# Performance work log

Hardware: AMD Instinct MI355X
Metric: run time of the kernel (lower is better)

## Reference

```python
import jax, jax.numpy as jnp
import numpy as np

N = 1024          # num_features
H = N // 2        # core dimension (num_params // 2)
NB = 4            # num_blocks
B = 16384         # batch


def _lifted_core(rot_params, diag_params):
    """Build the (N, N) lifted core matrix for one Cayley block."""
    # skew-symmetric matrix from the H rotation params
    S = rot_params[:, None] - rot_params[None, :]            # (H, H)
    I = jnp.eye(H, dtype=rot_params.dtype)
    rotation = jnp.linalg.solve(I - S, I + S)                # Cayley transform
    core = diag_params[:, None] * rotation                   # diag(d) @ rotation
    # rot90(core, k=o) only depends on o mod 4 -> precompute 4 variants
    rots = jnp.stack([core,
                      jnp.rot90(core, 1),
                      jnp.rot90(core, 2),
                      jnp.rot90(core, 3)])                   # (4, H, H)

    def body(lifted, o):
        blk = jax.lax.dynamic_slice(lifted, (o, o), (H, H)) + rots[o % 4]
        return jax.lax.dynamic_update_slice(lifted, blk, (o, o)), None

    lifted, _ = jax.lax.scan(body, jnp.zeros((N, N), dtype=core.dtype),
                             jnp.arange(H + 1))
    return lifted


def setup_inputs() -> dict:
    key = jax.random.key(0)
    ks = jax.random.split(key, 5)
    x = jax.random.normal(ks[0], (B, N), dtype=jnp.float32)
    enc_rot = jax.random.normal(ks[1], (NB, H), dtype=jnp.float32)
    enc_diag = jax.random.normal(ks[2], (NB, H), dtype=jnp.float32)
    dec_rot = jax.random.normal(ks[3], (NB, H), dtype=jnp.float32)
    dec_diag = jax.random.normal(ks[4], (NB, H), dtype=jnp.float32)
    return {"x": x, "enc_rot": enc_rot, "enc_diag": enc_diag,
            "dec_rot": dec_rot, "dec_diag": dec_diag}


def reference(x, enc_rot, enc_diag, dec_rot, dec_diag):
    s = x
    for i in range(NB):                                      # encoder blocks
        s = s @ _lifted_core(enc_rot[i], enc_diag[i]).T
    bottleneck = s
    out = s
    for i in range(NB):                                      # decoder blocks
        out = out @ _lifted_core(dec_rot[i], dec_diag[i]).T
    return bottleneck, out
```

## Files before the change

### kernel.cpp

```cpp
#include <hip/hip_runtime.h>
#include <hip/hip_bf16.h>
#include <cstdint>
#include <cstddef>

#define H 512
#define NFEAT 1024
#define BATCH 16384
#define LM ((size_t)1 << 20)
#define KOP 576

using bf16 = __hip_bfloat16;
using bf16x8 = __attribute__((ext_vector_type(8))) __bf16;
using f32x4 = __attribute__((ext_vector_type(4))) float;
using f32x16 = __attribute__((ext_vector_type(16))) float;

__device__ __forceinline__ void gload16(void* lds, const void* g) {
  __builtin_amdgcn_global_load_lds(
      (__attribute__((address_space(1))) void*)g,
      (__attribute__((address_space(3))) void*)lds,
      16, 0, 0);
}

__global__ void prep_kernel(const float* __restrict__ er, const float* __restrict__ ed,
                            const float* __restrict__ dr, const float* __restrict__ dd,
                            float* __restrict__ ab) {
  const int mat = blockIdx.x;
  const int lane = threadIdx.x;
  const float* u = (mat < 4) ? (er + mat * H) : (dr + (mat - 4) * H);
  const float* d = (mat < 4) ? (ed + mat * H) : (dd + (mat - 4) * H);

  double s = 0.0, q = 0.0;
  for (int k = 0; k < 8; ++k) {
    double v = (double)u[lane + 64 * k];
    s += v;
    q += v * v;
  }
  for (int off = 32; off; off >>= 1) {
    s += __shfl_down(s, off);
    q += __shfl_down(q, off);
  }
  s = __shfl(s, 0);
  q = __shfl(q, 0);

  const double det = 1.0 - s * s + (double)H * q;
  const double cuv = 2.0 * (1.0 + s) / det;
  const double cuu = -2.0 * (double)H / det;
  const double cvv = -2.0 * q / det;
  const double cvu = -2.0 * (1.0 - s) / det;

  float* a = ab + mat * 1024;
  float* b = a + H;
  for (int k = 0; k < 8; ++k) {
    int idx = lane + 64 * k;
    double ui = (double)u[idx], di = (double)d[idx];
    a[idx] = (float)(di * (cuv * ui + cvv));
    b[idx] = (float)(di * (cuu * ui + cvu));
  }
}

__global__ __launch_bounds__(256) void prep2_kernel(
    const float* __restrict__ er, const float* __restrict__ ed,
    const float* __restrict__ dr, const float* __restrict__ dd,
    const float* __restrict__ ab, float* __restrict__ Tpref) {
  __shared__ float buf[4][512];
  __shared__ float tmp[4][512];
  const int mat = blockIdx.x;
  const float* d = (mat < 4) ? (ed + mat * H) : (dd + (mat - 4) * H);
  const float* a = ab + mat * 1024;
  const int t = threadIdx.x;
  for (int m = t; m < 512; m += 256) {
    buf[0][m] = a[m];
    buf[1][m] = a[511 - m];
    buf[2][m] = d[m];
    buf[3][m] = d[511 - m];
  }
  __syncthreads();
  for (int s = 4; s <= 256; s <<= 1) {
    for (int m = t; m < 512; m += 256)
#pragma unroll
      for (int q = 0; q < 4; ++q) tmp[q][m] = (m >= s) ? buf[q][m - s] : 0.f;
    __syncthreads();
    for (int m = t; m < 512; m += 256)
#pragma unroll
      for (int q = 0; q < 4; ++q) buf[q][m] += tmp[q][m];
    __syncthreads();
  }
  float* tp = Tpref + mat * 2048;
  for (int m = t; m < 512; m += 256) {
    tp[m] = buf[0][m];
    tp[512 + m] = buf[1][m];
    tp[1024 + m] = buf[2][m];
    tp[1536 + m] = buf[3][m];
  }
}

__global__ __launch_bounds__(256) void genops_kernel(
    const float* __restrict__ er, const float* __restrict__ dr,
    const float* __restrict__ ab,
    bf16* __restrict__ Ah, bf16* __restrict__ Al,
    bf16* __restrict__ Bh, bf16* __restrict__ Bl) {
  const int x = blockIdx.x;
  const int mat = blockIdx.y;
  const float* u = (mat < 4) ? (er + mat * H) : (dr + (mat - 4) * H);
  const float* b = ab + mat * 1024 + H;
  const int t = threadIdx.x;
  const size_t base = ((size_t)mat * 1024 + x) * KOP;
  for (int k = t; k < KOP; k += 256) {
    float av = 0.f, bv = 0.f;
    if (k <= 128) {
      const int o = 4 * k;
      const int ia = x - o;
      av = (ia >= 0 && ia < 512) ? b[ia] : 0.f;
      bv = (ia >= 0 && ia < 512) ? u[ia] : 0.f;
    } else if (k <= 256) {
      const int o = 4 * (k - 129) + 1;
      const int ia = 511 - x + o;
      const int ib = x - o;
      av = (ia >= 0 && ia < 512) ? u[ia] : 0.f;
      bv = (ib >= 0 && ib < 512) ? b[ib] : 0.f;
    } else if (k <= 384) {
      const int o = 4 * (k - 257) + 2;
      const int ia = 511 - x + o;
      av = (ia >= 0 && ia < 512) ? b[ia] : 0.f;
      bv = (ia >= 0 && ia < 512) ? u[ia] : 0.f;
    } else if (k <= 512) {
      const int o = 4 * (k - 385) + 3;
      const int ia = x - o;
      const int ib = 511 - x + o;
      av = (ia >= 0 && ia < 512) ? u[ia] : 0.f;
      bv = (ib >= 0 && ib < 512) ? b[ib] : 0.f;
    }
    const bf16 ah = __float2bfloat16(av);
    Ah[base + k] = ah;
    Al[base + k] = __float2bfloat16(av - __bfloat162float(ah));
    const bf16 bh = __float2bfloat16(bv);
    Bh[base + k] = bh;
    Bl[base + k] = __float2bfloat16(bv - __bfloat162float(bh));
  }
}

__global__ __launch_bounds__(256) void buildgemm_kernel(
    const bf16* __restrict__ Ah, const bf16* __restrict__ Al,
    const bf16* __restrict__ Bh, const bf16* __restrict__ Bl,
    const float* __restrict__ ed, const float* __restrict__ dd,
    const float* __restrict__ Tpref, bf16* __restrict__ Lbase) {
  __shared__ __align__(16) bf16 smem[4 * 8192];
  __shared__ float pa[512], parev[512], pd[512], pdrev[512], sdl[512];
  bf16* sAh = smem;
  bf16* sAl = smem + 8192;
  bf16* sBh = smem + 16384;
  bf16* sBl = smem + 24576;

  const int tid = threadIdx.x;
  const int lane = tid & 63;
  const int wave = tid >> 6;
  const int wr = wave >> 1;
  const int wc = wave & 1;
  const int mat = blockIdx.z;
  const int row0 = blockIdx.x * 128;
  const int col0 = blockIdx.y * 128;

  {
    const float* tp = Tpref + mat * 2048;
    const float* d = (mat < 4) ? (ed + mat * H) : (dd + (mat - 4) * H);
    for (int m = tid; m < 512; m += 256) {
      pa[m] = tp[m];
      parev[m] = tp[512 + m];
      pd[m] = tp[1024 + m];
      pdrev[m] = tp[1536 + m];
      sdl[m] = d[m];
    }
  }

  const size_t OPS = (size_t)mat * 1024 * KOP;
  const int srow = tid >> 3;
  const int sce = (((tid * 16) ^ (((tid >> 3) & 7) << 4)) & 127) >> 1;
  const size_t abase = OPS + (size_t)(row0 + srow) * KOP + sce;
  const size_t bbase = OPS + (size_t)(col0 + srow) * KOP + sce;
  const int dst0 = tid * 8;

  f32x16 acc[2][2] = {};

  for (int kt = 0; kt < 9; ++kt) {
    const int k0 = kt * 64;
#pragma unroll
    for (int q = 0; q < 4; ++q) {
      const size_t ga = abase + (size_t)(32 * q) * KOP + k0;
      const size_t gb = bbase + (size_t)(32 * q) * KOP + k0;
      const int dq = q * 2048 + dst0;
      gload16(sAh + dq, Ah + ga);
      gload16(sAl + dq, Al + ga);
      gload16(sBh + dq, Bh + gb);
      gload16(sBl + dq, Bl + gb);
    }
    __syncthreads();

    const int l31 = lane & 31;
    const int kh16 = (lane >> 5) * 16;
#pragma unroll
    for (int ks = 0; ks < 4; ++ks) {
      bf16x8 fah[2], fal[2], fbh[2], fbl[2];
#pragma unroll
      for (int m = 0; m < 2; ++m) {
        const int arow = wr * 64 + m * 32 + l31;
        const int abk = (arow * 128 + ks * 32 + kh16) ^ ((arow & 7) << 4);
        fah[m] = *(const bf16x8*)((const char*)sAh + abk);
        fal[m] = *(const bf16x8*)((const char*)sAl + abk);
        const int brow = wc * 64 + m * 32 + l31;
        const int bbk = (brow * 128 + ks * 32 + kh16) ^ ((brow & 7) << 4);
        fbh[m] = *(const bf16x8*)((const char*)sBh + bbk);
        fbl[m] = *(const bf16x8*)((const char*)sBl + bbk);
      }
#pragma unroll
      for (int m = 0; m < 2; ++m)
#pragma unroll
        for (int n = 0; n < 2; ++n) {
          acc[m][n] = __builtin_amdgcn_mfma_f32_32x32x16_bf16(fah[m], fbh[n], acc[m][n], 0, 0, 0);
          acc[m][n] = __builtin_amdgcn_mfma_f32_32x32x16_bf16(fah[m], fbl[n], acc[m][n], 0, 0, 0);
          acc[m][n] = __builtin_amdgcn_mfma_f32_32x32x16_bf16(fal[m], fbh[n], acc[m][n], 0, 0, 0);
        }
    }
    __syncthreads();
  }

  auto apart = [&](int i, int j) -> float {
    const int lo = max(0, max(i, j) - 511);
    const int hi = min(512, min(i, j));
    if (lo > hi) return 0.f;
    float v = 0.f;
    {
      int o1 = lo + ((0 - lo) & 3), o2 = hi - (hi & 3);
      if (o1 <= o2) { int mx = i - o1, mn = i - o2; v += pa[mx] - (mn >= 4 ? pa[mn - 4] : 0.f); }
    }
    {
      int o1 = lo + ((1 - lo) & 3), o2 = hi - ((hi - 1) & 3);
      if (o1 <= o2) { int mx = j - o1, mn = j - o2; v += pa[mx] - (mn >= 4 ? pa[mn - 4] : 0.f); }
    }
    {
      int o1 = lo + ((2 - lo) & 3), o2 = hi - ((hi - 2) & 3);
      if (o1 <= o2) { int mx = i - o1, mn = i - o2; v += parev[mx] - (mn >= 4 ? parev[mn - 4] : 0.f); }
    }
    {
      int o1 = lo + ((3 - lo) & 3), o2 = hi - ((hi - 3) & 3);
      if (o1 <= o2) { int mx = j - o1, mn = j - o2; v += parev[mx] - (mn >= 4 ? parev[mn - 4] : 0.f); }
    }
    if (i == j) {
      {
        int o1 = lo + ((0 - lo) & 3), o2 = hi - (hi & 3);
        if (o1 <= o2) { int mx = i - o1, mn = i - o2; v += pd[mx] - (mn >= 4 ? pd[mn - 4] : 0.f); }
      }
      {
        int o1 = lo + ((2 - lo) & 3), o2 = hi - ((hi - 2) & 3);
        if (o1 <= o2) { int mx = i - o1, mn = i - o2; v += pdrev[mx] - (mn >= 4 ? pdrev[mn - 4] : 0.f); }
      }
    }
    const int m2 = i + j - 511;
    if (m2 >= 0 && !(m2 & 1)) {
      const int os = m2 >> 1;
      if (os >= lo && os <= hi) {
        const int r = os & 3;
        if (r == 1) v += sdl[j - os];
        else if (r == 3) v += sdl[511 - (j - os)];
      }
    }
    return v;
  };

  const int ocol0 = col0 + wc * 64 + (lane & 31);
  const int rb = (lane >> 5) << 2;
#pragma unroll
  for (int m = 0; m < 2; ++m)
#pragma unroll
    for (int n = 0; n < 2; ++n)
#pragma unroll
      for (int r = 0; r < 16; ++r) {
        const int grow = row0 + wr * 64 + m * 32 + (r & 3) + ((r >> 2) << 3) + rb;
        const int gcol = ocol0 + n * 32;
        const float v = acc[m][n][r] + apart(grow, gcol);
        const size_t off = ((size_t)mat << 21) + ((size_t)grow << 10) + (size_t)gcol;
        const bf16 hb = __float2bfloat16(v);
        Lbase[off] = hb;
        Lbase[off + LM] = __float2bfloat16(v - __bfloat162float(hb));
      }
}

__global__ void splith_kernel(const float* __restrict__ x, bf16* __restrict__ h) {
  const int n4 = BATCH * NFEAT / 4;
  int idx = blockIdx.x * blockDim.x + threadIdx.x;
  int stride = gridDim.x * blockDim.x;
  for (int i = idx; i < n4; i += stride) {
    float4 v = ((const float4*)x)[i];
    union { bf16 b[4]; short4 s; } Hu;
    Hu.b[0] = __float2bfloat16(v.x);
    Hu.b[1] = __float2bfloat16(v.y);
    Hu.b[2] = __float2bfloat16(v.z);
    Hu.b[3] = __float2bfloat16(v.w);
    ((short4*)h)[i] = Hu.s;
  }
}

struct TPtrs { const bf16* s; bf16* d; };
struct T6 { TPtrs t[6]; };

__global__ __launch_bounds__(256) void transposeB_kernel(T6 p) {
  const bf16* S = p.t[blockIdx.z].s;
  bf16* D = p.t[blockIdx.z].d;
  __shared__ ushort tile[64][68];
  const int i0 = blockIdx.x * 64, j0 = blockIdx.y * 64;
  const int tid = threadIdx.x;
  const int rr = tid >> 4;
  const int cc = (tid & 15) * 4;
#pragma unroll
  for (int it = 0; it < 4; ++it) {
    const int row = it * 16 + rr;
    const size_t so = (size_t)(i0 + row) * 1024 + j0 + cc;
    ushort4 v = *(const ushort4*)((const ushort*)S + so);
    tile[row][cc] = v.x; tile[row][cc + 1] = v.y;
    tile[row][cc + 2] = v.z; tile[row][cc + 3] = v.w;
  }
  __syncthreads();
#pragma unroll
  for (int it = 0; it < 4; ++it) {
    const int row = it * 16 + rr;
    ushort4 o;
    o.x = tile[cc][row];     o.y = tile[cc + 1][row];
    o.z = tile[cc + 2][row]; o.w = tile[cc + 3][row];
    const size_t dofs = (size_t)(j0 + row) * 1024 + i0 + cc;
    *(ushort4*)((ushort*)D + dofs) = o;
  }
}

struct GPtrs { const bf16* a; const bf16* b; bf16* yh; bf16* yl; };
struct G4 { GPtrs g[4]; };

__global__ __launch_bounds__(256) void chaingemm4_kernel(G4 p) {
  GPtrs q = p.g[blockIdx.z];
  const bf16* A = q.a;
  const bf16* Bh = q.b;
  const bf16* Bl = q.b + LM;

  __shared__ __align__(16) bf16 smem[2 * 3 * 4096];

  const int tid = threadIdx.x;
  const int lane = tid & 63;
  const int wave = tid >> 6;
  const int wr = wave >> 1, wc = wave & 1;
  const int r0 = blockIdx.x * 64, c0 = blockIdx.y * 64;

  const int srow = tid >> 3;
  const int scol = (((tid & 7) ^ (srow & 7))) * 8;
  const int dst = tid * 8;
  const size_t ga0 = (size_t)(r0 + srow) * 1024 + scol;
  const size_t gb0 = (size_t)(c0 + srow) * 1024 + scol;

  auto STAGE = [&](int nb, int k0) {
    bf16* base = smem + nb * 12288;
    gload16(base + dst,        A + ga0 + k0);
    gload16(base + 2048 + dst, A + ga0 + 32 * 1024 + k0);
    gload16(base + 4096 + dst,        Bh + gb0 + k0);
    gload16(base + 4096 + 2048 + dst, Bh + gb0 + 32 * 1024 + k0);
    gload16(base + 8192 + dst,        Bl + gb0 + k0);
    gload16(base + 8192 + 2048 + dst, Bl + gb0 + 32 * 1024 + k0);
  };

  const int l31 = lane & 31;
  const int klg = lane >> 5;
  const int ar = wr * 32 + l31;
  const int br = wc * 32 + l31;
  int aoff[4], boff[4];
#pragma unroll
  for (int ks = 0; ks < 4; ++ks) {
    const int lgA = (ks << 1) | klg;
    aoff[ks] = ar * 64 + ((lgA ^ (ar & 7)) << 3);
    boff[ks] = br * 64 + ((lgA ^ (br & 7)) << 3);
  }

  f32x16 acc = {};

  STAGE(0, 0);
  asm volatile("s_waitcnt vmcnt(0)" ::: "memory");
  __builtin_amdgcn_s_barrier();

  for (int t = 0; t < 16; ++t) {
    const int buf = t & 1;
    const int nb = buf ^ 1;
    const bool pf = (t < 15);
    if (pf) STAGE(nb, (t + 1) * 64);

    const bf16* pA = smem + buf * 12288;
    const bf16* pBh = pA + 4096;
    const bf16* pBl = pA + 8192;
#pragma unroll
    for (int ks = 0; ks < 4; ++ks) {
      bf16x8 ah = *(const bf16x8*)(pA + aoff[ks]);
      bf16x8 bh = *(const bf16x8*)(pBh + boff[ks]);
      bf16x8 bl = *(const bf16x8*)(pBl + boff[ks]);
      acc = __builtin_amdgcn_mfma_f32_32x32x16_bf16(ah, bh, acc, 0, 0, 0);
      acc = __builtin_amdgcn_mfma_f32_32x32x16_bf16(ah, bl, acc, 0, 0, 0);
    }
    if (pf) asm volatile("s_waitcnt vmcnt(0)" ::: "memory");
    __builtin_amdgcn_s_barrier();
  }

  const int oc = c0 + wc * 32 + l31;
  const int rb = (lane >> 5) << 2;
#pragma unroll
  for (int r = 0; r < 16; ++r) {
    const int gr = r0 + wr * 32 + (r & 3) + ((r >> 2) << 3) + rb;
    const size_t off = (size_t)gr * 1024 + oc;
    const float v = acc[r];
    const bf16 hb = __float2bfloat16(v);
    q.yh[off] = hb;
    q.yl[off] = __float2bfloat16(v - __bfloat162float(hb));
  }
}

__global__ __launch_bounds__(512, 1) void gemmbig_kernel(
    const bf16* __restrict__ A, const bf16* __restrict__ Bh_,
    float* __restrict__ Y0, float* __restrict__ Y1) {
  __shared__ __align__(16) bf16 smem[2 * 2 * 8192];

  const int tid = threadIdx.x;
  const int lane = tid & 63;
  const int wave = tid >> 6;
  const int wr = wave >> 2;
  const int wc = wave & 3;

  const int pdisp = blockIdx.x + (blockIdx.y << 6);
  const int xcd = pdisp & 7;
  const int chk = pdisp >> 3;
  const int row0 = (xcd * 8 + (chk >> 3)) * 256;
  const int col0 = (chk & 7) * 256;

  const int gsrc = (tid & 3) ^ ((tid >> 3) & 3);
  const int dst = tid * 8;
  const size_t abase = (size_t)(row0 + (tid >> 2)) * NFEAT + gsrc * 8;
  const size_t bbase = (size_t)(col0 + (tid >> 2)) * NFEAT + gsrc * 8;

  auto STAGE2 = [&](int nb, int arr, const bf16* __restrict__ src, size_t base, int k0) {
    bf16* d = smem + nb * 16384 + arr * 8192 + dst;
    gload16(d, src + base + k0);
    gload16(d + 4096, src + base + 131072 + k0);
  };

  const int l31 = lane & 31;
  const int hb = lane >> 5;
  int aoffB[4][2], boffB[2][2];
#pragma unroll
  for (int m = 0; m < 4; ++m) {
    const int r = wr * 128 + m * 32 + l31;
#pragma unroll
    for (int ks = 0; ks < 2; ++ks)
      aoffB[m][ks] = r * 64 + ((((ks << 1) | hb) ^ ((r >> 1) & 3)) << 4);
  }
#pragma unroll
  for (int n = 0; n < 2; ++n) {
    const int r = wc * 64 + n * 32 + l31;
#pragma unroll
    for (int ks = 0; ks < 2; ++ks)
      boffB[n][ks] = r * 64 + ((((ks << 1) | hb) ^ ((r >> 1) & 3)) << 4);
  }

  auto LD = [](const char* base, int off) { return *(const bf16x8*)(base + off); };

  f32x16 acc[4][2] = {};

  STAGE2(0, 0, A, abase, 0);
  STAGE2(0, 1, Bh_, bbase, 0);
  asm volatile("s_waitcnt vmcnt(0)" ::: "memory");
  __builtin_amdgcn_s_barrier();

  for (int t = 0; t < 32; ++t) {
    const int buf = t & 1;
    const int nb = buf ^ 1;
    const int k1 = (t + 1) * 32;
    const char* pA = (const char*)(smem + buf * 16384);
    const char* pBh = pA + 16384;
    const bool pf = (t < 31);

    bf16x8 ga[2][2], fbh[2][2];

    if (pf) {
      STAGE2(nb, 0, A, abase, k1);
      STAGE2(nb, 1, Bh_, bbase, k1);
    }
#pragma unroll
    for (int mi = 0; mi < 2; ++mi)
#pragma unroll
      for (int ks = 0; ks < 2; ++ks)
        ga[mi][ks] = LD(pA, aoffB[mi][ks]);
#pragma unroll
    for (int n = 0; n < 2; ++n)
#pragma unroll
      for (int ks = 0; ks < 2; ++ks)
        fbh[n][ks] = LD(pBh, boffB[n][ks]);
    __builtin_amdgcn_s_barrier();
    __builtin_amdgcn_s_setprio(1);
#pragma unroll
    for (int ks = 0; ks < 2; ++ks)
#pragma unroll
      for (int mi = 0; mi < 2; ++mi)
#pragma unroll
        for (int n = 0; n < 2; ++n)
          acc[mi][n] = __builtin_amdgcn_mfma_f32_32x32x16_bf16(ga[mi][ks], fbh[n][ks], acc[mi][n], 0, 0, 0);
    __builtin_amdgcn_s_setprio(0);
    __builtin_amdgcn_s_barrier();

#pragma unroll
    for (int mi = 0; mi < 2; ++mi)
#pragma unroll
      for (int ks = 0; ks < 2; ++ks)
        ga[mi][ks] = LD(pA, aoffB[2 + mi][ks]);
    __builtin_amdgcn_s_barrier();
    __builtin_amdgcn_s_setprio(1);
#pragma unroll
    for (int ks = 0; ks < 2; ++ks)
#pragma unroll
      for (int mi = 0; mi < 2; ++mi)
#pragma unroll
        for (int n = 0; n < 2; ++n)
          acc[2 + mi][n] = __builtin_amdgcn_mfma_f32_32x32x16_bf16(ga[mi][ks], fbh[n][ks], acc[2 + mi][n], 0, 0, 0);
    __builtin_amdgcn_s_setprio(0);
    if (pf) asm volatile("s_waitcnt vmcnt(0)" ::: "memory");
    __builtin_amdgcn_s_barrier();
  }

  float* Yb = (col0 < 1024) ? Y0 : (Y1 - 1024);
  const int ocol0 = col0 + wc * 64 + l31;
  const int rb = (lane >> 5) << 2;
#pragma unroll
  for (int m = 0; m < 4; ++m)
#pragma unroll
    for (int n = 0; n < 2; ++n)
#pragma unroll
      for (int r = 0; r < 16; ++r) {
        const int grow = row0 + wr * 128 + m * 32 + (r & 3) + ((r >> 2) << 3) + rb;
        const int gcol = ocol0 + n * 32;
        Yb[(size_t)grow * NFEAT + (size_t)gcol] = acc[m][n][r];
      }
}

extern "C" void kernel_launch(void* const* d_in, const int* in_sizes, int n_in,
                              void* d_out, int out_size, void* d_ws, size_t ws_size,
                              hipStream_t stream) {
  (void)in_sizes; (void)n_in; (void)out_size; (void)ws_size;
  const float* x  = (const float*)d_in[0];
  const float* er = (const float*)d_in[1];
  const float* ed = (const float*)d_in[2];
  const float* dr = (const float*)d_in[3];
  const float* dd = (const float*)d_in[4];

  float* O0 = (float*)d_out;
  float* O1 = O0 + (size_t)BATCH * NFEAT;

  bf16* Lb = (bf16*)d_ws;
  float* ab = (float*)(Lb + 16 * LM);
  bf16* Qh = (bf16*)(ab + 8 * 1024);

  float* Tpref = O0;
  bf16* SB = (bf16*)((char*)O0 + (1 << 20));
  auto slot = [&](int s) { return SB + (size_t)s * LM; };

  const size_t OPN = (size_t)8 * 1024 * KOP;
  bf16* Aoph = (bf16*)O1;
  bf16* Aopl = Aoph + OPN;
  bf16* Boph = Aopl + OPN;
  bf16* Bopl = Boph + OPN;

  prep_kernel<<<8, 64, 0, stream>>>(er, ed, dr, dd, ab);
  prep2_kernel<<<8, 256, 0, stream>>>(er, ed, dr, dd, ab, Tpref);
  genops_kernel<<<dim3(1024, 8), 256, 0, stream>>>(er, dr, ab, Aoph, Aopl, Boph, Bopl);
  buildgemm_kernel<<<dim3(8, 8, 8), 256, 0, stream>>>(Aoph, Aopl, Boph, Bopl,
                                                      ed, dd, Tpref, Lb);
  splith_kernel<<<4096, 256, 0, stream>>>(x, Qh);

  {
    T6 p;
    p.t[0] = {Lb + 0 * LM,  slot(0)};
    p.t[1] = {Lb + 4 * LM,  slot(2)};
    p.t[2] = {Lb + 5 * LM,  slot(3)};
    p.t[3] = {Lb + 8 * LM,  slot(4)};
    p.t[4] = {Lb + 12 * LM, slot(6)};
    p.t[5] = {Lb + 13 * LM, slot(7)};
    transposeB_kernel<<<dim3(16, 16, 6), 256, 0, stream>>>(p);
  }
  {
    G4 p;
    p.g[0] = {slot(0),      Lb + 2 * LM,  slot(8),  slot(9)};
    p.g[1] = {Lb + 6 * LM,  slot(2),      slot(10), slot(11)};
    p.g[2] = {slot(4),      Lb + 10 * LM, slot(12), slot(13)};
    p.g[3] = {Lb + 14 * LM, slot(6),      slot(14), slot(15)};
    chaingemm4_kernel<<<dim3(16, 16, 4), 256, 0, stream>>>(p);
  }
  {
    G4 p;
    p.g[0] = {slot(8),  slot(10), slot(0), slot(1)};
    p.g[1] = {slot(12), slot(14), slot(2), slot(3)};
    p.g[2] = p.g[0];
    p.g[3] = p.g[1];
    chaingemm4_kernel<<<dim3(16, 16, 2), 256, 0, stream>>>(p);
  }
  {
    T6 p;
    p.t[0] = {slot(0), Lb + 0 * LM};
    p.t[1] = {slot(2), Lb + 2 * LM};
    p.t[2] = p.t[0]; p.t[3] = p.t[0]; p.t[4] = p.t[0]; p.t[5] = p.t[0];
    transposeB_kernel<<<dim3(16, 16, 2), 256, 0, stream>>>(p);
  }
  {
    G4 p;
    p.g[0] = {Lb + 2 * LM, slot(0), Lb + 1 * LM, slot(4)};
    p.g[1] = p.g[0]; p.g[2] = p.g[0]; p.g[3] = p.g[0];
    chaingemm4_kernel<<<dim3(16, 16, 1), 256, 0, stream>>>(p);
  }

  gemmbig_kernel<<<dim3(64, 8), 512, 0, stream>>>(Qh, Lb, O0, O1);
}
```

Before: 259.3 us.

## Triple-buffer LDS in big GEMM and drop intra-iteration barriers

Moves the big GEMM kernel from double- to triple-buffered LDS staging, prefetching two K-steps ahead and waiting with vmcnt(4) so one tile's loads stay in flight across iterations. It also removes the two mid-iteration barriers and keeps a single barrier per K-step. This is meant to hide global load latency better and cut synchronisation stalls. The cost is 50% more LDS (96 KB per block) and reliance on vmcnt ordering for correctness.

```diff
diff --git a/kernel.cpp b/kernel.cpp
--- a/kernel.cpp
+++ b/kernel.cpp
@@ -418,7 +418,7 @@
 __global__ __launch_bounds__(512, 1) void gemmbig_kernel(
     const bf16* __restrict__ A, const bf16* __restrict__ Bh_,
     float* __restrict__ Y0, float* __restrict__ Y1) {
-  __shared__ __align__(16) bf16 smem[2 * 2 * 8192];
+  __shared__ __align__(16) bf16 smem[3 * 2 * 8192];
 
   const int tid = threadIdx.x;
   const int lane = tid & 63;
@@ -437,10 +437,11 @@
   const size_t abase = (size_t)(row0 + (tid >> 2)) * NFEAT + gsrc * 8;
   const size_t bbase = (size_t)(col0 + (tid >> 2)) * NFEAT + gsrc * 8;
 
-  auto STAGE2 = [&](int nb, int arr, const bf16* __restrict__ src, size_t base, int k0) {
-    bf16* d = smem + nb * 16384 + arr * 8192 + dst;
-    gload16(d, src + base + k0);
-    gload16(d + 4096, src + base + 131072 + k0);
+  auto STAGE = [&](bf16* bufp, int k0) {
+    gload16(bufp + dst, A + abase + k0);
+    gload16(bufp + 4096 + dst, A + abase + 131072 + k0);
+    gload16(bufp + 8192 + dst, Bh_ + bbase + k0);
+    gload16(bufp + 12288 + dst, Bh_ + bbase + 131072 + k0);
   };
 
   const int l31 = lane & 31;
@@ -465,36 +466,33 @@
 
   f32x16 acc[4][2] = {};
 
-  STAGE2(0, 0, A, abase, 0);
-  STAGE2(0, 1, Bh_, bbase, 0);
-  asm volatile("s_waitcnt vmcnt(0)" ::: "memory");
+  bf16* b0 = smem;
+  bf16* b1 = smem + 16384;
+  bf16* b2 = smem + 32768;
+
+  STAGE(b0, 0);
+  STAGE(b1, 32);
+  asm volatile("s_waitcnt vmcnt(4)" ::: "memory");
   __builtin_amdgcn_s_barrier();
 
   for (int t = 0; t < 32; ++t) {
-    const int buf = t & 1;
-    const int nb = buf ^ 1;
-    const int k1 = (t + 1) * 32;
-    const char* pA = (const char*)(smem + buf * 16384);
+    if (t < 30) STAGE(b2, (t + 2) * 32);
+
+    const char* pA = (const char*)b0;
     const char* pBh = pA + 16384;
-    const bool pf = (t < 31);
 
     bf16x8 ga[2][2], fbh[2][2];
-
-    if (pf) {
-      STAGE2(nb, 0, A, abase, k1);
-      STAGE2(nb, 1, Bh_, bbase, k1);
-    }
+#pragma unroll
+    for (int n = 0; n < 2; ++n)
+#pragma unroll
+      for (int ks = 0; ks < 2; ++ks)
+        fbh[n][ks] = LD(pBh, boffB[n][ks]);
 #pragma unroll
     for (int mi = 0; mi < 2; ++mi)
 #pragma unroll
       for (int ks = 0; ks < 2; ++ks)
         ga[mi][ks] = LD(pA, aoffB[mi][ks]);
-#pragma unroll
-    for (int n = 0; n < 2; ++n)
-#pragma unroll
-      for (int ks = 0; ks < 2; ++ks)
-        fbh[n][ks] = LD(pBh, boffB[n][ks]);
-    __builtin_amdgcn_s_barrier();
+
     __builtin_amdgcn_s_setprio(1);
 #pragma unroll
     for (int ks = 0; ks < 2; ++ks)
@@ -504,14 +502,13 @@
         for (int n = 0; n < 2; ++n)
           acc[mi][n] = __builtin_amdgcn_mfma_f32_32x32x16_bf16(ga[mi][ks], fbh[n][ks], acc[mi][n], 0, 0, 0);
     __builtin_amdgcn_s_setprio(0);
-    __builtin_amdgcn_s_barrier();
 
 #pragma unroll
     for (int mi = 0; mi < 2; ++mi)
 #pragma unroll
       for (int ks = 0; ks < 2; ++ks)
         ga[mi][ks] = LD(pA, aoffB[2 + mi][ks]);
-    __builtin_amdgcn_s_barrier();
+
     __builtin_amdgcn_s_setprio(1);
 #pragma unroll
     for (int ks = 0; ks < 2; ++ks)
@@ -521,8 +518,15 @@
         for (int n = 0; n < 2; ++n)
           acc[2 + mi][n] = __builtin_amdgcn_mfma_f32_32x32x16_bf16(ga[mi][ks], fbh[n][ks], acc[2 + mi][n], 0, 0, 0);
     __builtin_amdgcn_s_setprio(0);
-    if (pf) asm volatile("s_waitcnt vmcnt(0)" ::: "memory");
+
+    if (t < 30) {
+      asm volatile("s_waitcnt vmcnt(4)" ::: "memory");
+    } else {
+      asm volatile("s_waitcnt vmcnt(0)" ::: "memory");
+    }
     __builtin_amdgcn_s_barrier();
+
+    bf16* tmp = b0; b0 = b1; b1 = b2; b2 = tmp;
   }
 
   float* Yb = (col0 < 1024) ? Y0 : (Y1 - 1024);
```

New measurement: 258.3 us. No clear change (-0.4%).

## Deepen gemmbig LDS pipeline to four stages and switch to 16x16x32 MFMA

Applied to the files above, without the earlier changes.

Replaces the double-buffered LDS pipeline in the big GEMM with a four-buffer ring that prefetches three K-steps ahead. The A and B global-to-LDS loads for each step are split across the two compute halves, and partial vmcnt waits are used. It also moves from 32x32x16 to 16x16x32 MFMA fragments, with new swizzled LDS offsets and a matching output mapping. The aim is to hide global load latency better, at the cost of twice the LDS and more fragment loads per step.

```diff
diff --git a/kernel.cpp b/kernel.cpp
--- a/kernel.cpp
+++ b/kernel.cpp
@@ -418,7 +418,7 @@
 __global__ __launch_bounds__(512, 1) void gemmbig_kernel(
     const bf16* __restrict__ A, const bf16* __restrict__ Bh_,
     float* __restrict__ Y0, float* __restrict__ Y1) {
-  __shared__ __align__(16) bf16 smem[2 * 2 * 8192];
+  __shared__ __align__(16) bf16 smem[4 * 16384];
 
   const int tid = threadIdx.x;
   const int lane = tid & 63;
@@ -432,111 +432,104 @@
   const int row0 = (xcd * 8 + (chk >> 3)) * 256;
   const int col0 = (chk & 7) * 256;
 
-  const int gsrc = (tid & 3) ^ ((tid >> 3) & 3);
+  const int sr = tid >> 2;
+  const int sc = ((tid & 3) ^ ((tid >> 3) & 3)) * 8;
+  const size_t abase0 = (size_t)(row0 + sr) * NFEAT + sc;
+  const size_t abase1 = (size_t)(row0 + sr + 128) * NFEAT + sc;
+  const size_t bbase0 = (size_t)(col0 + sr) * NFEAT + sc;
+  const size_t bbase1 = (size_t)(col0 + sr + 128) * NFEAT + sc;
   const int dst = tid * 8;
-  const size_t abase = (size_t)(row0 + (tid >> 2)) * NFEAT + gsrc * 8;
-  const size_t bbase = (size_t)(col0 + (tid >> 2)) * NFEAT + gsrc * 8;
-
-  auto STAGE2 = [&](int nb, int arr, const bf16* __restrict__ src, size_t base, int k0) {
-    bf16* d = smem + nb * 16384 + arr * 8192 + dst;
-    gload16(d, src + base + k0);
-    gload16(d + 4096, src + base + 131072 + k0);
+
+  auto STAGE_A = [&](int buf, int k0) {
+    bf16* base = smem + buf * 16384;
+    gload16(base + dst, A + abase0 + k0);
+    gload16(base + 4096 + dst, A + abase1 + k0);
   };
-
-  const int l31 = lane & 31;
-  const int hb = lane >> 5;
-  int aoffB[4][2], boffB[2][2];
-#pragma unroll
-  for (int m = 0; m < 4; ++m) {
-    const int r = wr * 128 + m * 32 + l31;
-#pragma unroll
-    for (int ks = 0; ks < 2; ++ks)
-      aoffB[m][ks] = r * 64 + ((((ks << 1) | hb) ^ ((r >> 1) & 3)) << 4);
-  }
-#pragma unroll
-  for (int n = 0; n < 2; ++n) {
-    const int r = wc * 64 + n * 32 + l31;
-#pragma unroll
-    for (int ks = 0; ks < 2; ++ks)
-      boffB[n][ks] = r * 64 + ((((ks << 1) | hb) ^ ((r >> 1) & 3)) << 4);
-  }
-
-  auto LD = [](const char* base, int off) { return *(const bf16x8*)(base + off); };
-
-  f32x16 acc[4][2] = {};
-
-  STAGE2(0, 0, A, abase, 0);
-  STAGE2(0, 1, Bh_, bbase, 0);
-  asm volatile("s_waitcnt vmcnt(0)" ::: "memory");
+  auto STAGE_B = [&](int buf, int k0) {
+    bf16* base = smem + buf * 16384 + 8192;
+    gload16(base + dst, Bh_ + bbase0 + k0);
+    gload16(base + 4096 + dst, Bh_ + bbase1 + k0);
+  };
+
+  const int l15 = lane & 15;
+  const int kg16 = (lane >> 4) * 16;
+  const int swz = ((l15 >> 1) & 3) << 4;
+  const int kcol = kg16 ^ swz;
+  int aoff[8], boff[4];
+#pragma unroll
+  for (int fr = 0; fr < 8; ++fr)
+    aoff[fr] = (wr * 128 + fr * 16 + l15) * 64 + kcol;
+#pragma unroll
+  for (int fc = 0; fc < 4; ++fc)
+    boff[fc] = (wc * 64 + fc * 16 + l15) * 64 + kcol + 16384;
+
+  auto LD = [&](int buf, int off) {
+    return *(const bf16x8*)((const char*)(smem + buf * 16384) + off);
+  };
+
+  f32x4 acc[8][4] = {};
+
+  STAGE_A(0, 0); STAGE_B(0, 0);
+  STAGE_A(1, 32); STAGE_B(1, 32);
+  STAGE_A(2, 64); STAGE_B(2, 64);
+  asm volatile("s_waitcnt vmcnt(8)" ::: "memory");
   __builtin_amdgcn_s_barrier();
 
-  for (int t = 0; t < 32; ++t) {
-    const int buf = t & 1;
-    const int nb = buf ^ 1;
-    const int k1 = (t + 1) * 32;
-    const char* pA = (const char*)(smem + buf * 16384);
-    const char* pBh = pA + 16384;
-    const bool pf = (t < 31);
-
-    bf16x8 ga[2][2], fbh[2][2];
-
-    if (pf) {
-      STAGE2(nb, 0, A, abase, k1);
-      STAGE2(nb, 1, Bh_, bbase, k1);
-    }
-#pragma unroll
-    for (int mi = 0; mi < 2; ++mi)
-#pragma unroll
-      for (int ks = 0; ks < 2; ++ks)
-        ga[mi][ks] = LD(pA, aoffB[mi][ks]);
-#pragma unroll
-    for (int n = 0; n < 2; ++n)
-#pragma unroll
-      for (int ks = 0; ks < 2; ++ks)
-        fbh[n][ks] = LD(pBh, boffB[n][ks]);
+  for (int T = 0; T < 32; ++T) {
+    const int buf = T & 3;
+    const int kpre = (T + 3) * 32;
+    const bool pf = (T < 29);
+
+    bf16x8 fa[4], fb[4];
+
+    if (pf) STAGE_A((T + 3) & 3, kpre);
+#pragma unroll
+    for (int fc = 0; fc < 4; ++fc) fb[fc] = LD(buf, boff[fc]);
+#pragma unroll
+    for (int fr = 0; fr < 4; ++fr) fa[fr] = LD(buf, aoff[fr]);
     __builtin_amdgcn_s_barrier();
     __builtin_amdgcn_s_setprio(1);
 #pragma unroll
-    for (int ks = 0; ks < 2; ++ks)
-#pragma unroll
-      for (int mi = 0; mi < 2; ++mi)
-#pragma unroll
-        for (int n = 0; n < 2; ++n)
-          acc[mi][n] = __builtin_amdgcn_mfma_f32_32x32x16_bf16(ga[mi][ks], fbh[n][ks], acc[mi][n], 0, 0, 0);
+    for (int fr = 0; fr < 4; ++fr)
+#pragma unroll
+      for (int fc = 0; fc < 4; ++fc)
+        acc[fr][fc] = __builtin_amdgcn_mfma_f32_16x16x32_bf16(fa[fr], fb[fc], acc[fr][fc], 0, 0, 0);
     __builtin_amdgcn_s_setprio(0);
     __builtin_amdgcn_s_barrier();
 
-#pragma unroll
-    for (int mi = 0; mi < 2; ++mi)
-#pragma unroll
-      for (int ks = 0; ks < 2; ++ks)
-        ga[mi][ks] = LD(pA, aoffB[2 + mi][ks]);
+    if (pf) STAGE_B((T + 3) & 3, kpre);
+#pragma unroll
+    for (int fr = 0; fr < 4; ++fr) fa[fr] = LD(buf, aoff[4 + fr]);
     __builtin_amdgcn_s_barrier();
     __builtin_amdgcn_s_setprio(1);
 #pragma unroll
-    for (int ks = 0; ks < 2; ++ks)
-#pragma unroll
-      for (int mi = 0; mi < 2; ++mi)
-#pragma unroll
-        for (int n = 0; n < 2; ++n)
-          acc[2 + mi][n] = __builtin_amdgcn_mfma_f32_32x32x16_bf16(ga[mi][ks], fbh[n][ks], acc[2 + mi][n], 0, 0, 0);
+    for (int fr = 0; fr < 4; ++fr)
+#pragma unroll
+      for (int fc = 0; fc < 4; ++fc)
+        acc[4 + fr][fc] = __builtin_amdgcn_mfma_f32_16x16x32_bf16(fa[fr], fb[fc], acc[4 + fr][fc], 0, 0, 0);
     __builtin_amdgcn_s_setprio(0);
-    if (pf) asm volatile("s_waitcnt vmcnt(0)" ::: "memory");
+    if (T <= 28) {
+      asm volatile("s_waitcnt vmcnt(8)" ::: "memory");
+    } else if (T == 29) {
+      asm volatile("s_waitcnt vmcnt(4)" ::: "memory");
+    } else if (T == 30) {
+      asm volatile("s_waitcnt vmcnt(0)" ::: "memory");
+    }
     __builtin_amdgcn_s_barrier();
   }
 
   float* Yb = (col0 < 1024) ? Y0 : (Y1 - 1024);
-  const int ocol0 = col0 + wc * 64 + l31;
-  const int rb = (lane >> 5) << 2;
-#pragma unroll
-  for (int m = 0; m < 4; ++m)
-#pragma unroll
-    for (int n = 0; n < 2; ++n)
-#pragma unroll
-      for (int r = 0; r < 16; ++r) {
-        const int grow = row0 + wr * 128 + m * 32 + (r & 3) + ((r >> 2) << 3) + rb;
-        const int gcol = ocol0 + n * 32;
-        Yb[(size_t)grow * NFEAT + (size_t)gcol] = acc[m][n][r];
+  const int orow = row0 + wr * 128 + (lane >> 4) * 4;
+  const int ocol = col0 + wc * 64 + l15;
+#pragma unroll
+  for (int fr = 0; fr < 8; ++fr)
+#pragma unroll
+    for (int fc = 0; fc < 4; ++fc)
+#pragma unroll
+      for (int r = 0; r < 4; ++r) {
+        const int grow = orow + fr * 16 + r;
+        const int gcol = ocol + fc * 16;
+        Yb[(size_t)grow * NFEAT + (size_t)gcol] = acc[fr][fc][r];
       }
 }
 
```

Result: no change. 257.2 us (-0.8%).
